# Optimization experiments

Measured on AMD Instinct MI355X. Metric: run time of the kernel, lower is better.

## Reference

```python
import jax, jax.numpy as jnp
import numpy as np

N = 50000   # nodes
E = 1600000 # edges (avg degree 32)
IN, D, OUT = 128, 256, 128
NUM_MID = 8  # num_layers - 2


def gcn_conv(x, W, b, src, dst, n):
    """PyG GCNConv: add self-loops, symmetric norm, linear transform, scatter-sum."""
    h = x @ W                                           # [n, d_out]
    ones = jnp.ones(src.shape[0], h.dtype)
    deg = jax.ops.segment_sum(ones, dst, num_segments=n) + 1.0  # +1 self-loop
    dinv = jax.lax.rsqrt(deg)                           # deg^{-1/2}
    coef = dinv[src] * dinv[dst]                        # [E]
    agg = jax.ops.segment_sum(h[src] * coef[:, None], dst, num_segments=n)
    agg = agg + h * (dinv * dinv)[:, None]              # self-loop term: dinv[i]^2
    return agg + b


def layer_norm(x, g, b, eps=1e-5):
    mu = jnp.mean(x, axis=-1, keepdims=True)
    var = jnp.mean(jnp.square(x - mu), axis=-1, keepdims=True)
    return (x - mu) * jax.lax.rsqrt(var + eps) * g + b


def setup_inputs() -> dict:
    key = jax.random.key(0)
    ks = jax.random.split(key, 8)
    x = jax.random.normal(ks[0], (N, IN), dtype=jnp.float32)
    edge_index = jax.random.randint(ks[1], (2, E), 0, N, dtype=jnp.int64)
    s_in = 1.0 / np.sqrt(IN)
    s_d = 1.0 / np.sqrt(D)
    return {
        "x": x,
        "edge_index": edge_index,
        "W_in": jax.random.normal(ks[2], (IN, D), dtype=jnp.float32) * s_in,
        "b_in": jnp.zeros((D,), jnp.float32),
        "W_mid": jax.random.normal(ks[3], (NUM_MID, D, D), dtype=jnp.float32) * s_d,
        "b_mid": jnp.zeros((NUM_MID, D), jnp.float32),
        "W_out": jax.random.normal(ks[4], (D, OUT), dtype=jnp.float32) * s_d,
        "b_out": jnp.zeros((OUT,), jnp.float32),
        "gamma": jnp.ones((NUM_MID + 1, D), jnp.float32),
        "beta": jnp.zeros((NUM_MID + 1, D), jnp.float32),
    }


def reference(x, edge_index, W_in, b_in, W_mid, b_mid, W_out, b_out, gamma, beta):
    # Inference mode: dropout is identity.
    src, dst = edge_index[0], edge_index[1]
    n = x.shape[0]
    h = gcn_conv(x, W_in, b_in, src, dst, n)
    h = jax.nn.silu(layer_norm(h, gamma[0], beta[0]))
    for i in range(NUM_MID):  # fixed small layer count
        h = gcn_conv(h, W_mid[i], b_mid[i], src, dst, n)
        h = jax.nn.silu(layer_norm(h, gamma[i + 1], beta[i + 1]))
    return gcn_conv(h, W_out, b_out, src, dst, n)
```

## Files before the change

### kernel.cpp

```cpp
#include <hip/hip_runtime.h>
#include <stdint.h>

#define NN   50000
#define NE   1600000
#define DIN  128
#define DMID 256
#define DOUT 128
#define NMID 8
#define MAXD 2048
#define NBIN 128
#define NBKB 196
#define NG16 3128
#define NNP  (NG16 * 16)
#define ECAP (NE + 64 * MAXD)

#define AS1 __attribute__((address_space(1)))
#define AS3 __attribute__((address_space(3)))

typedef unsigned short u16;
typedef unsigned int   u32;
typedef __attribute__((ext_vector_type(8))) short short8;
typedef __attribute__((ext_vector_type(4))) float f32x4;
typedef __attribute__((ext_vector_type(2))) float f32x2;
typedef __attribute__((ext_vector_type(4))) int i32x4;

__device__ __forceinline__ float bf2f(u32 u) {
    union { u32 i; float f; } c; c.i = u << 16; return c.f;
}
__device__ __forceinline__ float ubf_lo(u32 v) {
    union { u32 i; float f; } c; c.i = v << 16; return c.f;
}
__device__ __forceinline__ float ubf_hi(u32 v) {
    union { u32 i; float f; } c; c.i = v & 0xffff0000u; return c.f;
}
__device__ __forceinline__ u16 f2bf(float f) {
    union { float f; u32 i; } c; c.f = f;
    u32 u = c.i;
    return (u16)((u + 0x7fffu + ((u >> 16) & 1u)) >> 16);
}
__device__ __forceinline__ void split2(float v, u16& hi, u16& lo) {
    hi = f2bf(v);
    float r = v - bf2f(hi);
    lo = f2bf(r);
}

__global__ void rank_kernel(const int* __restrict__ ei, int* __restrict__ counts,
                            int* __restrict__ rank) {
    int i = (blockIdx.x * blockDim.x + threadIdx.x) * 4;
    if (i < NE) {
        i32x4 d = *(const i32x4*)(ei + NE + i);
        i32x4 r;
        r.x = atomicAdd(&counts[d.x], 1);
        r.y = atomicAdd(&counts[d.y], 1);
        r.z = atomicAdd(&counts[d.z], 1);
        r.w = atomicAdd(&counts[d.w], 1);
        *(i32x4*)(rank + i) = r;
    }
}


__global__ __launch_bounds__(256) void hist2_kernel(const int* __restrict__ counts,
                                                    int* __restrict__ bcnt) {
    __shared__ int h[NBIN];
    const int t = threadIdx.x;
    if (t < NBIN) h[t] = 0;
    __syncthreads();
    int i = blockIdx.x * 256 + t;
    if (i < NN) {
        int d = counts[i];
        atomicAdd(&h[d < NBIN ? d : NBIN - 1], 1);
    }
    __syncthreads();
    if (t < NBIN) bcnt[blockIdx.x * NBIN + t] = h[t];
}

__global__ __launch_bounds__(128) void bscan_kernel(const int* __restrict__ bcnt,
                                                    int* __restrict__ bbase) {
    __shared__ int B[NBIN];
    const int b = threadIdx.x;
    int run = 0;
    for (int k = 0; k < NBKB; ++k) {
        bbase[k * NBIN + b] = run;
        run += bcnt[k * NBIN + b];
    }
    __shared__ int S[NBIN];
    S[b] = run;
    __syncthreads();
    if (b == 0) {
        int acc = 0;
        for (int x = NBIN - 1; x >= 0; --x) { B[x] = acc; acc += S[x]; }
    }
    __syncthreads();
    const int add = B[b];
    for (int k = 0; k < NBKB; ++k) bbase[k * NBIN + b] += add;
}

__global__ __launch_bounds__(256) void psort2_kernel(const int* __restrict__ counts,
                                                     const int* __restrict__ bbase,
                                                     int* __restrict__ perm,
                                                     int* __restrict__ posv,
                                                     int* __restrict__ degp,
                                                     float* __restrict__ dinv) {
    __shared__ int h[NBIN];
    const int t = threadIdx.x;
    if (t < NBIN) h[t] = 0;
    __syncthreads();
    int i = blockIdx.x * 256 + t;
    int d = 0, b = 0, r = 0;
    if (i < NN) {
        d = counts[i];
        b = d < NBIN ? d : NBIN - 1;
        r = atomicAdd(&h[b], 1);
    }
    __syncthreads();
    if (i < NN) {
        int pos = bbase[blockIdx.x * NBIN + b] + r;
        perm[pos] = i;
        posv[i] = pos;
        degp[pos] = d;
        dinv[i] = rsqrtf((float)d + 1.0f);
    }
}

__global__ void ptail_kernel(int* __restrict__ perm, int* __restrict__ degp) {
    int i = NN + threadIdx.x;
    if (i < NNP) { perm[i] = NN; degp[i] = 0; }
}

__global__ void gcap_kernel(const int* __restrict__ degp, int* __restrict__ gcap) {
    int g = blockIdx.x * blockDim.x + threadIdx.x;
    if (g < NG16) {
        int m = 0;
        for (int j = 0; j < 16; ++j) {
            int d = degp[g * 16 + j];
            m = d > m ? d : m;
        }
        gcap[g] = m;
    }
}

__global__ __launch_bounds__(1024) void gscan_kernel(const int* __restrict__ gcap,
                                                     int* __restrict__ gbase) {
    __shared__ int sh[1024];
    const int t = threadIdx.x;
    int loc[4];
    int s = 0;
#pragma unroll
    for (int j = 0; j < 4; ++j) {
        int idx = t * 4 + j;
        int v = (idx < NG16) ? gcap[idx] * 16 : 0;
        loc[j] = s;
        s += v;
    }
    sh[t] = s;
    __syncthreads();
    for (int offs = 1; offs < 1024; offs <<= 1) {
        int x = (t >= offs) ? sh[t - offs] : 0;
        __syncthreads();
        sh[t] += x;
        __syncthreads();
    }
    int base = (t == 0) ? 0 : sh[t - 1];
#pragma unroll
    for (int j = 0; j < 4; ++j) {
        int idx = t * 4 + j;
        if (idx < NG16) gbase[idx] = base + loc[j];
    }
}

__global__ void escat_kernel(const int* __restrict__ ei, const int* __restrict__ rank,
                             const int* __restrict__ posv, const int* __restrict__ gbase,
                             u16* __restrict__ esrc) {
    int i = (blockIdx.x * blockDim.x + threadIdx.x) * 4;
    if (i < NE) {
        i32x4 d = *(const i32x4*)(ei + NE + i);
        i32x4 s = *(const i32x4*)(ei + i);
        i32x4 r = *(const i32x4*)(rank + i);
        { int p = posv[d.x]; esrc[gbase[p >> 4] + r.x * 16 + (p & 15)] = (u16)s.x; }
        { int p = posv[d.y]; esrc[gbase[p >> 4] + r.y * 16 + (p & 15)] = (u16)s.y; }
        { int p = posv[d.z]; esrc[gbase[p >> 4] + r.z * 16 + (p & 15)] = (u16)s.z; }
        { int p = posv[d.w]; esrc[gbase[p >> 4] + r.w * 16 + (p & 15)] = (u16)s.w; }
    }
}

__global__ void zsent_kernel(u16* __restrict__ gs) {
    int s = threadIdx.x >> 5, c = threadIdx.x & 31;
    gs[((size_t)s * (NN + 1) + NN) * 32 + c] = 0;
}

__global__ void wsplit_kernel(const float* __restrict__ W, u16* __restrict__ Whi,
                              u16* __restrict__ Wlo, int K, int Dc) {
    int idx = blockIdx.x * blockDim.x + threadIdx.x;
    if (idx < K * Dc) {
        int k = idx / Dc, d = idx - k * Dc;
        u16 hi, lo;
        split2(W[idx], hi, lo);
        size_t o = ((size_t)(k >> 5) * Dc + d) * 32 + (k & 31);
        Whi[o] = hi;
        Wlo[o] = lo;
    }
}

__global__ void xsplit_kernel(const float* __restrict__ x, u16* __restrict__ xhi,
                              u16* __restrict__ xlo) {
    int i = blockIdx.x * blockDim.x + threadIdx.x;
    int stride = gridDim.x * blockDim.x;
    for (; i < NN * DIN; i += stride) {
        u16 hi, lo;
        split2(x[i], hi, lo);
        xhi[i] = hi;
        xlo[i] = lo;
    }
}

template <int K, int Dc>
__global__ __launch_bounds__(512, 4) void gemm_kernel(const u16* __restrict__ xhi,
                                                      const u16* __restrict__ xlo,
                                                      const u16* __restrict__ whi,
                                                      const u16* __restrict__ wlo,
                                                      const float* __restrict__ dinv,
                                                      u16* __restrict__ gs) {
    constexpr int NTW = Dc / 32;
    constexpr int KS = K / 32;
    __shared__ u16 bh[Dc * 32];
    __shared__ u16 bl[Dc * 32];
    const int tid = threadIdx.x;
    const int wid = tid >> 6;
    const int rowPanel = wid >> 1;
    const int colPanel = wid & 1;
    const int lane = tid & 63;
    const int m = lane & 15, quad = lane >> 4;
    const int rowBase = blockIdx.x * 128 + rowPanel * 32;

    f32x4 acc[2][NTW];
#pragma unroll
    for (int rg = 0; rg < 2; ++rg)
#pragma unroll
        for (int t = 0; t < NTW; ++t) acc[rg][t] = (f32x4){0.f, 0.f, 0.f, 0.f};

    size_t arow[2];
#pragma unroll
    for (int rg = 0; rg < 2; ++rg) {
        int rowA = rowBase + rg * 16 + m;
        if (rowA > NN - 1) rowA = NN - 1;
        arow[rg] = (size_t)rowA * K + quad * 8;
    }

    for (int ks = 0; ks < KS; ++ks) {
        const u16* sh_src = whi + (size_t)ks * Dc * 32;
        const u16* sl_src = wlo + (size_t)ks * Dc * 32;
        __syncthreads();
#pragma unroll
        for (int i = 0; i < Dc * 4; i += 512) {
            int j = i + tid;
            __builtin_amdgcn_global_load_lds((const AS1 void*)(sh_src + j * 8),
                                             (AS3 void*)((AS3 u16*)bh + j * 8), 16, 0, 0);
            __builtin_amdgcn_global_load_lds((const AS1 void*)(sl_src + j * 8),
                                             (AS3 void*)((AS3 u16*)bl + j * 8), 16, 0, 0);
        }
        short8 ah[2], al[2];
#pragma unroll
        for (int rg = 0; rg < 2; ++rg) {
            ah[rg] = *(const short8*)(xhi + arow[rg] + ks * 32);
            al[rg] = *(const short8*)(xlo + arow[rg] + ks * 32);
        }
        __syncthreads();
#pragma unroll
        for (int t = 0; t < NTW; ++t) {
            const int bo = ((colPanel * NTW + t) * 16 + m) * 32 + quad * 8;
            short8 wh = *(const short8*)(bh + bo);
            short8 wl = *(const short8*)(bl + bo);
#pragma unroll
            for (int rg = 0; rg < 2; ++rg) {
                acc[rg][t] = __builtin_amdgcn_mfma_f32_16x16x32_bf16(ah[rg], wh, acc[rg][t], 0, 0, 0);
                acc[rg][t] = __builtin_amdgcn_mfma_f32_16x16x32_bf16(al[rg], wh, acc[rg][t], 0, 0, 0);
                acc[rg][t] = __builtin_amdgcn_mfma_f32_16x16x32_bf16(ah[rg], wl, acc[rg][t], 0, 0, 0);
            }
        }
    }

#pragma unroll
    for (int rg = 0; rg < 2; ++rg) {
        const int r0 = rowBase + rg * 16 + quad * 4;
        float dv[4];
#pragma unroll
        for (int r = 0; r < 4; ++r) {
            int rr = r0 + r;
            dv[r] = (rr < NN) ? dinv[rr] : 0.f;
        }
#pragma unroll
        for (int t = 0; t < NTW; ++t) {
            const int col = colPanel * (Dc / 2) + t * 16 + m;
#pragma unroll
            for (int r = 0; r < 4; ++r) {
                int rr = r0 + r;
                if (rr < NN) {
                    size_t o = ((size_t)(col >> 5) * (NN + 1) + rr) * 32 + (col & 31);
                    gs[o] = f2bf(acc[rg][t][r] * dv[r]);
                }
            }
        }
    }
}


template <int Dc, bool FINAL>
__global__ __launch_bounds__(256, 8) void agg_kernel(const u16* __restrict__ gs,
                                                     const u16* __restrict__ esrc,
                                                     const int* __restrict__ gbase,
                                                     const int* __restrict__ perm,
                                                     const int* __restrict__ degp,
                                                     const float* __restrict__ dinv,
                                                     const float* __restrict__ bias,
                                                     float* __restrict__ vs,
                                                     float* __restrict__ part,
                                                     float* __restrict__ outf) {
    constexpr int NSL = Dc / 32;
    constexpr int SH = (NSL == 8) ? 3 : 2;
    const int slice = blockIdx.x & (NSL - 1);
    const int grp4 = blockIdx.x >> SH;
    const int wid = threadIdx.x >> 6, lane = threadIdx.x & 63;
    const int grp = grp4 * 4 + wid;
    const int nslot = lane >> 2, q = lane & 3;
    const int gpos = grp * 16 + nslot;
    const int node = perm[gpos];
    const int deg = degp[gpos];

    const u16* gslb = gs + (size_t)slice * (NN + 1) * 32 + q * 8;
    const u16* ep = esrc + gbase[grp] + nslot;

    float a[8];
#pragma unroll
    for (int j = 0; j < 8; ++j) a[j] = 0.f;

    uint4 A = *(const uint4*)(gslb + (size_t)node * 32);
    int sNxt = (deg > 0) ? (int)ep[0] : node;
    int t = 0;
    for (;;) {
        uint4 B = *(const uint4*)(gslb + (size_t)sNxt * 32);
        int sN2 = (t + 1 < deg) ? (int)ep[(t + 1) * 16] : sNxt;
        a[0] += ubf_lo(A.x); a[1] += ubf_hi(A.x);
        a[2] += ubf_lo(A.y); a[3] += ubf_hi(A.y);
        a[4] += ubf_lo(A.z); a[5] += ubf_hi(A.z);
        a[6] += ubf_lo(A.w); a[7] += ubf_hi(A.w);
        ++t;
        if (t > deg) break;
        A = B;
        sNxt = sN2;
    }

    if (node < NN) {
        const float dv = dinv[node];
        const int f = slice * 32 + q * 8;
        float v[8];
        f32x4 b0 = *(const f32x4*)(bias + f);
        f32x4 b1 = *(const f32x4*)(bias + f + 4);
#pragma unroll
        for (int j = 0; j < 4; ++j) v[j] = a[j] * dv + b0[j];
#pragma unroll
        for (int j = 0; j < 4; ++j) v[j + 4] = a[j + 4] * dv + b1[j];

        if (FINAL) {
            float* op = outf + (size_t)node * Dc + f;
            *(f32x4*)op = (f32x4){v[0], v[1], v[2], v[3]};
            *(f32x4*)(op + 4) = (f32x4){v[4], v[5], v[6], v[7]};
        } else {
            float* vp = vs + ((size_t)slice * NN + node) * 32 + q * 8;
            *(f32x4*)vp = (f32x4){v[0], v[1], v[2], v[3]};
            *(f32x4*)(vp + 4) = (f32x4){v[4], v[5], v[6], v[7]};
            float p1 = 0.f, p2 = 0.f;
#pragma unroll
            for (int j = 0; j < 8; ++j) {
                p1 += v[j];
                p2 += v[j] * v[j];
            }
            p1 += __shfl_xor(p1, 1, 64); p2 += __shfl_xor(p2, 1, 64);
            p1 += __shfl_xor(p1, 2, 64); p2 += __shfl_xor(p2, 2, 64);
            if (q == 0)
                *(f32x2*)(part + ((size_t)slice * NN + node) * 2) = (f32x2){p1, p2};
        }
    }
}

__global__ __launch_bounds__(256) void ln_kernel(const float* __restrict__ vs,
                                                 const float* __restrict__ part,
                                                 const float* __restrict__ gamma,
                                                 const float* __restrict__ beta,
                                                 u16* __restrict__ xhi,
                                                 u16* __restrict__ xlo) {
    const int wid = threadIdx.x >> 6, lane = threadIdx.x & 63;
    const int node = blockIdx.x * 4 + wid;
    const int s = lane >> 3, o = (lane & 7) * 4;

    f32x4 vv = *(const f32x4*)(vs + ((size_t)s * NN + node) * 32 + o);
    f32x2 p = *(const f32x2*)(part + ((size_t)(lane & 7) * NN + node) * 2);
    float s1 = p.x, s2 = p.y;
    s1 += __shfl_xor(s1, 1, 64); s2 += __shfl_xor(s2, 1, 64);
    s1 += __shfl_xor(s1, 2, 64); s2 += __shfl_xor(s2, 2, 64);
    s1 += __shfl_xor(s1, 4, 64); s2 += __shfl_xor(s2, 4, 64);

    const float mu = s1 * (1.f / 256.f);
    const float var = s2 * (1.f / 256.f) - mu * mu;
    const float rstd = rsqrtf(fmaxf(var, 0.f) + 1e-5f);

    const int f = s * 32 + o;
    u16 hh[4], ll[4];
#pragma unroll
    for (int j = 0; j < 4; ++j) {
        float y = (vv[j] - mu) * rstd * gamma[f + j] + beta[f + j];
        y = y / (1.f + __expf(-y));
        split2(y, hh[j], ll[j]);
    }
    uint2 oh, ol;
    oh.x = (u32)hh[0] | ((u32)hh[1] << 16);
    oh.y = (u32)hh[2] | ((u32)hh[3] << 16);
    ol.x = (u32)ll[0] | ((u32)ll[1] << 16);
    ol.y = (u32)ll[2] | ((u32)ll[3] << 16);
    *(uint2*)(xhi + (size_t)node * 256 + f) = oh;
    *(uint2*)(xlo + (size_t)node * 256 + f) = ol;
}


extern "C" void kernel_launch(void* const* d_in, const int* in_sizes, int n_in,
                              void* d_out, int out_size, void* d_ws, size_t ws_size,
                              hipStream_t stream) {
    (void)in_sizes; (void)n_in; (void)out_size; (void)ws_size;
    const float* x_in  = (const float*)d_in[0];
    const int*   ei    = (const int*)d_in[1];
    const float* W_in  = (const float*)d_in[2];
    const float* b_in  = (const float*)d_in[3];
    const float* W_mid = (const float*)d_in[4];
    const float* b_mid = (const float*)d_in[5];
    const float* W_out = (const float*)d_in[6];
    const float* b_out = (const float*)d_in[7];
    const float* gamma = (const float*)d_in[8];
    const float* beta  = (const float*)d_in[9];

    char* ws = (char*)d_ws;
    size_t off = 0;
    auto alloc = [&](size_t bytes) -> char* {
        char* p = ws + off;
        off += (bytes + 255) & ~(size_t)255;
        return p;
    };
    float* dinv   = (float*)alloc((size_t)NN * 4);
    int* counts   = (int*)alloc((size_t)NN * 4);
    int* rank     = (int*)alloc((size_t)NE * 4);
    int* bcnt     = (int*)alloc((size_t)NBKB * NBIN * 4);
    int* bbase    = (int*)alloc((size_t)NBKB * NBIN * 4);
    int* perm     = (int*)alloc((size_t)NNP * 4);
    int* posv     = (int*)alloc((size_t)NN * 4);
    int* degp     = (int*)alloc((size_t)NNP * 4);
    int* gcap     = (int*)alloc((size_t)NG16 * 4);
    int* gbase    = (int*)alloc((size_t)NG16 * 4);
    u16* esrc     = (u16*)alloc((size_t)ECAP * 2);
    u16* whi_in   = (u16*)alloc((size_t)DIN * DMID * 2);
    u16* wlo_in   = (u16*)alloc((size_t)DIN * DMID * 2);
    u16* whi_mid  = (u16*)alloc((size_t)NMID * DMID * DMID * 2);
    u16* wlo_mid  = (u16*)alloc((size_t)NMID * DMID * DMID * 2);
    u16* whi_out  = (u16*)alloc((size_t)DMID * DOUT * 2);
    u16* wlo_out  = (u16*)alloc((size_t)DMID * DOUT * 2);
    u16* xhi      = (u16*)alloc((size_t)NN * DMID * 2);
    u16* xlo      = (u16*)alloc((size_t)NN * DMID * 2);
    u16* gs       = (u16*)alloc((size_t)8 * (NN + 1) * 32 * 2);
    float* vs     = (float*)alloc((size_t)NN * DMID * 4);
    float* part   = (float*)alloc((size_t)8 * NN * 2 * 4);

    hipMemsetAsync(counts, 0, (size_t)NN * 4, stream);

    const int EB4 = (NE / 4 + 255) / 256;
    rank_kernel<<<EB4, 256, 0, stream>>>(ei, counts, rank);
    hist2_kernel<<<NBKB, 256, 0, stream>>>(counts, bcnt);
    bscan_kernel<<<1, 128, 0, stream>>>(bcnt, bbase);
    psort2_kernel<<<NBKB, 256, 0, stream>>>(counts, bbase, perm, posv, degp, dinv);
    ptail_kernel<<<1, 64, 0, stream>>>(perm, degp);
    gcap_kernel<<<(NG16 + 255) / 256, 256, 0, stream>>>(degp, gcap);
    gscan_kernel<<<1, 1024, 0, stream>>>(gcap, gbase);
    escat_kernel<<<EB4, 256, 0, stream>>>(ei, rank, posv, gbase, esrc);
    zsent_kernel<<<1, 256, 0, stream>>>(gs);

    wsplit_kernel<<<(DIN * DMID + 255) / 256, 256, 0, stream>>>(W_in, whi_in, wlo_in, DIN, DMID);
    for (int i = 0; i < NMID; ++i)
        wsplit_kernel<<<(DMID * DMID + 255) / 256, 256, 0, stream>>>(
            W_mid + (size_t)i * DMID * DMID, whi_mid + (size_t)i * DMID * DMID,
            wlo_mid + (size_t)i * DMID * DMID, DMID, DMID);
    wsplit_kernel<<<(DMID * DOUT + 255) / 256, 256, 0, stream>>>(W_out, whi_out, wlo_out, DMID, DOUT);
    xsplit_kernel<<<1024, 256, 0, stream>>>(x_in, xhi, xlo);

    const int GB = (NN + 127) / 128;
    const int AGM = (NG16 / 4) * 8;
    const int AGF = (NG16 / 4) * 4;
    const int LNB = NN / 4;

    gemm_kernel<DIN, DMID><<<GB, 512, 0, stream>>>(xhi, xlo, whi_in, wlo_in, dinv, gs);
    agg_kernel<DMID, false><<<AGM, 256, 0, stream>>>(gs, esrc, gbase, perm, degp,
                                                     dinv, b_in, vs, part, nullptr);
    ln_kernel<<<LNB, 256, 0, stream>>>(vs, part, gamma, beta, xhi, xlo);
    for (int i = 0; i < NMID; ++i) {
        gemm_kernel<DMID, DMID><<<GB, 512, 0, stream>>>(xhi, xlo,
                                                        whi_mid + (size_t)i * DMID * DMID,
                                                        wlo_mid + (size_t)i * DMID * DMID,
                                                        dinv, gs);
        agg_kernel<DMID, false><<<AGM, 256, 0, stream>>>(gs, esrc, gbase, perm, degp,
                                                         dinv, b_mid + (size_t)i * DMID,
                                                         vs, part, nullptr);
        ln_kernel<<<LNB, 256, 0, stream>>>(vs, part,
                                           gamma + (size_t)(i + 1) * DMID,
                                           beta + (size_t)(i + 1) * DMID, xhi, xlo);
    }
    gemm_kernel<DMID, DOUT><<<GB, 512, 0, stream>>>(xhi, xlo, whi_out, wlo_out, dinv, gs);
    agg_kernel<DOUT, true><<<AGF, 256, 0, stream>>>(gs, esrc, gbase, perm, degp,
                                                    dinv, b_out, nullptr, nullptr,
                                                    (float*)d_out);
}
```

Baseline: 1.487 ms.

## Pad CSR groups to multiples of eight and unroll gather with deep prefetch

Each 16-node group's edge capacity is rounded up to a multiple of 8 (minimum 8). Padding slots are pre-filled with the sentinel node NN, whose gs row is zero. The aggregation loop now walks the group capacity uniformly and keeps 8 row loads in flight with double-buffered index prefetch, replacing the old one-ahead loop driven by per-node degree. This trades extra padded loads and a fill kernel for much more memory-level parallelism in the latency-bound gather.

```diff
diff --git a/kernel.cpp b/kernel.cpp
--- a/kernel.cpp
+++ b/kernel.cpp
@@ -12,7 +12,7 @@
 #define NBKB 196
 #define NG16 3128
 #define NNP  (NG16 * 16)
-#define ECAP (NE + 64 * MAXD)
+#define ECAP (NE + 64 * MAXD + 256 * NG16)
 
 #define AS1 __attribute__((address_space(1)))
 #define AS3 __attribute__((address_space(3)))
@@ -135,6 +135,8 @@
             int d = degp[g * 16 + j];
             m = d > m ? d : m;
         }
+        m = (m + 7) & ~7;
+        if (m < 8) m = 8;
         gcap[g] = m;
     }
 }
@@ -165,6 +167,14 @@
     for (int j = 0; j < 4; ++j) {
         int idx = t * 4 + j;
         if (idx < NG16) gbase[idx] = base + loc[j];
+    }
+}
+
+__global__ void efill_kernel(u16* __restrict__ esrc) {
+    int i = (blockIdx.x * blockDim.x + threadIdx.x) * 8;
+    if (i < ECAP) {
+        const int v = NN | (NN << 16);
+        *(i32x4*)(esrc + i) = (i32x4){v, v, v, v};
     }
 }
 
@@ -304,12 +314,18 @@
 }
 
 
+#define CONSROW(X) do { \
+    a[0] += ubf_lo((X).x); a[1] += ubf_hi((X).x); \
+    a[2] += ubf_lo((X).y); a[3] += ubf_hi((X).y); \
+    a[4] += ubf_lo((X).z); a[5] += ubf_hi((X).z); \
+    a[6] += ubf_lo((X).w); a[7] += ubf_hi((X).w); } while (0)
+
 template <int Dc, bool FINAL>
 __global__ __launch_bounds__(256, 8) void agg_kernel(const u16* __restrict__ gs,
                                                      const u16* __restrict__ esrc,
                                                      const int* __restrict__ gbase,
+                                                     const int* __restrict__ gcap,
                                                      const int* __restrict__ perm,
-                                                     const int* __restrict__ degp,
                                                      const float* __restrict__ dinv,
                                                      const float* __restrict__ bias,
                                                      float* __restrict__ vs,
@@ -324,7 +340,7 @@
     const int nslot = lane >> 2, q = lane & 3;
     const int gpos = grp * 16 + nslot;
     const int node = perm[gpos];
-    const int deg = degp[gpos];
+    const int nt = gcap[grp];
 
     const u16* gslb = gs + (size_t)slice * (NN + 1) * 32 + q * 8;
     const u16* ep = esrc + gbase[grp] + nslot;
@@ -333,32 +349,62 @@
 #pragma unroll
     for (int j = 0; j < 8; ++j) a[j] = 0.f;
 
-    uint4 A = *(const uint4*)(gslb + (size_t)node * 32);
-    int sNxt = (deg > 0) ? (int)ep[0] : node;
-    int t = 0;
+    int a0 = (int)ep[0],   a1 = (int)ep[16],  a2 = (int)ep[32],  a3 = (int)ep[48];
+    int b0 = (int)ep[64],  b1 = (int)ep[80],  b2 = (int)ep[96],  b3 = (int)ep[112];
+    uint4 RS = *(const uint4*)(gslb + (size_t)node * 32);
+    uint4 A0 = *(const uint4*)(gslb + (size_t)a0 * 32);
+    uint4 A1 = *(const uint4*)(gslb + (size_t)a1 * 32);
+    uint4 A2 = *(const uint4*)(gslb + (size_t)a2 * 32);
+    uint4 A3 = *(const uint4*)(gslb + (size_t)a3 * 32);
+    uint4 B0 = *(const uint4*)(gslb + (size_t)b0 * 32);
+    uint4 B1 = *(const uint4*)(gslb + (size_t)b1 * 32);
+    uint4 B2 = *(const uint4*)(gslb + (size_t)b2 * 32);
+    uint4 B3 = *(const uint4*)(gslb + (size_t)b3 * 32);
+    CONSROW(RS);
+    if (8 < nt) {
+        a0 = (int)ep[128]; a1 = (int)ep[144]; a2 = (int)ep[160]; a3 = (int)ep[176];
+    }
+    if (12 < nt) {
+        b0 = (int)ep[192]; b1 = (int)ep[208]; b2 = (int)ep[224]; b3 = (int)ep[240];
+    }
+
+    int c = 0;
     for (;;) {
-        uint4 B = *(const uint4*)(gslb + (size_t)sNxt * 32);
-        int sN2 = (t + 1 < deg) ? (int)ep[(t + 1) * 16] : sNxt;
-        a[0] += ubf_lo(A.x); a[1] += ubf_hi(A.x);
-        a[2] += ubf_lo(A.y); a[3] += ubf_hi(A.y);
-        a[4] += ubf_lo(A.z); a[5] += ubf_hi(A.z);
-        a[6] += ubf_lo(A.w); a[7] += ubf_hi(A.w);
-        ++t;
-        if (t > deg) break;
-        A = B;
-        sNxt = sN2;
+        CONSROW(A0); CONSROW(A1); CONSROW(A2); CONSROW(A3);
+        if ((c + 2) * 4 >= nt) {
+            CONSROW(B0); CONSROW(B1); CONSROW(B2); CONSROW(B3);
+            break;
+        }
+        A0 = *(const uint4*)(gslb + (size_t)a0 * 32);
+        A1 = *(const uint4*)(gslb + (size_t)a1 * 32);
+        A2 = *(const uint4*)(gslb + (size_t)a2 * 32);
+        A3 = *(const uint4*)(gslb + (size_t)a3 * 32);
+        if ((c + 4) * 4 < nt) {
+            const u16* sp = ep + (size_t)(c + 4) * 64;
+            a0 = (int)sp[0]; a1 = (int)sp[16]; a2 = (int)sp[32]; a3 = (int)sp[48];
+        }
+        CONSROW(B0); CONSROW(B1); CONSROW(B2); CONSROW(B3);
+        B0 = *(const uint4*)(gslb + (size_t)b0 * 32);
+        B1 = *(const uint4*)(gslb + (size_t)b1 * 32);
+        B2 = *(const uint4*)(gslb + (size_t)b2 * 32);
+        B3 = *(const uint4*)(gslb + (size_t)b3 * 32);
+        if ((c + 5) * 4 < nt) {
+            const u16* sp = ep + (size_t)(c + 5) * 64;
+            b0 = (int)sp[0]; b1 = (int)sp[16]; b2 = (int)sp[32]; b3 = (int)sp[48];
+        }
+        c += 2;
     }
 
     if (node < NN) {
         const float dv = dinv[node];
         const int f = slice * 32 + q * 8;
         float v[8];
-        f32x4 b0 = *(const f32x4*)(bias + f);
-        f32x4 b1 = *(const f32x4*)(bias + f + 4);
-#pragma unroll
-        for (int j = 0; j < 4; ++j) v[j] = a[j] * dv + b0[j];
-#pragma unroll
-        for (int j = 0; j < 4; ++j) v[j + 4] = a[j + 4] * dv + b1[j];
+        f32x4 bb0 = *(const f32x4*)(bias + f);
+        f32x4 bb1 = *(const f32x4*)(bias + f + 4);
+#pragma unroll
+        for (int j = 0; j < 4; ++j) v[j] = a[j] * dv + bb0[j];
+#pragma unroll
+        for (int j = 0; j < 4; ++j) v[j + 4] = a[j + 4] * dv + bb1[j];
 
         if (FINAL) {
             float* op = outf + (size_t)node * Dc + f;
@@ -476,6 +522,7 @@
     ptail_kernel<<<1, 64, 0, stream>>>(perm, degp);
     gcap_kernel<<<(NG16 + 255) / 256, 256, 0, stream>>>(degp, gcap);
     gscan_kernel<<<1, 1024, 0, stream>>>(gcap, gbase);
+    efill_kernel<<<(ECAP / 8 + 255) / 256, 256, 0, stream>>>(esrc);
     escat_kernel<<<EB4, 256, 0, stream>>>(ei, rank, posv, gbase, esrc);
     zsent_kernel<<<1, 256, 0, stream>>>(gs);
 
@@ -493,7 +540,7 @@
     const int LNB = NN / 4;
 
     gemm_kernel<DIN, DMID><<<GB, 512, 0, stream>>>(xhi, xlo, whi_in, wlo_in, dinv, gs);
-    agg_kernel<DMID, false><<<AGM, 256, 0, stream>>>(gs, esrc, gbase, perm, degp,
+    agg_kernel<DMID, false><<<AGM, 256, 0, stream>>>(gs, esrc, gbase, gcap, perm,
                                                      dinv, b_in, vs, part, nullptr);
     ln_kernel<<<LNB, 256, 0, stream>>>(vs, part, gamma, beta, xhi, xlo);
     for (int i = 0; i < NMID; ++i) {
@@ -501,7 +548,7 @@
                                                         whi_mid + (size_t)i * DMID * DMID,
                                                         wlo_mid + (size_t)i * DMID * DMID,
                                                         dinv, gs);
-        agg_kernel<DMID, false><<<AGM, 256, 0, stream>>>(gs, esrc, gbase, perm, degp,
+        agg_kernel<DMID, false><<<AGM, 256, 0, stream>>>(gs, esrc, gbase, gcap, perm,
                                                          dinv, b_mid + (size_t)i * DMID,
                                                          vs, part, nullptr);
         ln_kernel<<<LNB, 256, 0, stream>>>(vs, part,
@@ -509,7 +556,7 @@
                                            beta + (size_t)(i + 1) * DMID, xhi, xlo);
     }
     gemm_kernel<DMID, DOUT><<<GB, 512, 0, stream>>>(xhi, xlo, whi_out, wlo_out, dinv, gs);
-    agg_kernel<DOUT, true><<<AGF, 256, 0, stream>>>(gs, esrc, gbase, perm, degp,
+    agg_kernel<DOUT, true><<<AGF, 256, 0, stream>>>(gs, esrc, gbase, gcap, perm,
                                                     dinv, b_out, nullptr, nullptr,
                                                     (float*)d_out);
 }
```

Measured after the change: 4.153 ms. +179.3%, slower.
